# Kernel tuning notes

Measured on AMD Instinct MI355X. Metric: run time of the kernel, lower is better.

Reference implementation:

```python
import jax, jax.numpy as jnp
import numpy as np


def _graph_conv(x, src, dst, W_rel, b_rel, W_root):
    # PyG GraphConv (aggr='add'): out = lin_rel(sum_{j->i} x_j) + lin_root(x_i)
    agg = jax.ops.segment_sum(x[src], dst, num_segments=x.shape[0])  # [N, d]
    return agg @ W_rel + b_rel + x @ W_root


def setup_inputs() -> dict:
    N, E, D, H, G = 50000, 800000, 128, 128, 256
    key = jax.random.key(0)
    ks = jax.random.split(key, 24)
    x = jax.random.normal(ks[0], (N, D), dtype=jnp.float32)
    edge_index = jax.random.randint(ks[1], (2, E), 0, N, dtype=jnp.int64)
    batch = jnp.sort(jax.random.randint(ks[2], (N,), 0, G, dtype=jnp.int64))
    inp = {"x": x, "edge_index": edge_index, "batch": batch, "num_graphs": G}
    dims = [(D, H), (H, H), (H, H), (H, H), (H, H)]
    for i, (din, dout) in enumerate(dims, 1):
        s = 1.0 / np.sqrt(din)
        inp[f"W_rel{i}"] = jax.random.normal(ks[3 * i], (din, dout), dtype=jnp.float32) * s
        inp[f"b_rel{i}"] = jax.random.normal(ks[3 * i + 1], (dout,), dtype=jnp.float32) * s
        inp[f"W_root{i}"] = jax.random.normal(ks[3 * i + 2], (din, dout), dtype=jnp.float32) * s
    inp["fc1_W"] = jax.random.normal(ks[18], (H, H), dtype=jnp.float32) / np.sqrt(H)
    inp["fc1_b"] = jax.random.normal(ks[19], (H,), dtype=jnp.float32) / np.sqrt(H)
    inp["fc2_W"] = jax.random.normal(ks[20], (H, 1), dtype=jnp.float32) / np.sqrt(H)
    inp["fc2_b"] = jax.random.normal(ks[21], (1,), dtype=jnp.float32) / np.sqrt(H)
    return inp


def reference(x, edge_index, batch, num_graphs,
              W_rel1, b_rel1, W_root1,
              W_rel2, b_rel2, W_root2,
              W_rel3, b_rel3, W_root3,
              W_rel4, b_rel4, W_root4,
              W_rel5, b_rel5, W_root5,
              fc1_W, fc1_b, fc2_W, fc2_b):
    src, dst = edge_index[0], edge_index[1]
    h = x
    for Wr, br, Wl in ((W_rel1, b_rel1, W_root1), (W_rel2, b_rel2, W_root2),
                       (W_rel3, b_rel3, W_root3), (W_rel4, b_rel4, W_root4),
                       (W_rel5, b_rel5, W_root5)):
        h = jax.nn.relu(_graph_conv(h, src, dst, Wr, br, Wl))
    # global_add_pool -> [num_graphs, H]
    g = jax.ops.segment_sum(h, batch, num_segments=num_graphs)
    g = jax.nn.relu(g @ fc1_W + fc1_b)
    # dropout is identity in eval mode
    return g @ fc2_W + fc2_b  # [num_graphs, 1]
```

## Files before the change

### kernel.cpp

```cpp
#include <hip/hip_runtime.h>
#include <hip/hip_bf16.h>

typedef __attribute__((ext_vector_type(4))) float f32x4;
typedef __attribute__((ext_vector_type(8))) _Float16 f16x8;
typedef __attribute__((ext_vector_type(4))) _Float16 f16x4;

#define CHUNK 4096
#define BSH 7
#define CAP 4096


__global__ __launch_bounds__(256) void cvt_kernel(const float* __restrict__ x,
                                                  _Float16* __restrict__ hp, int N) {
  int i = blockIdx.x * blockDim.x + threadIdx.x;
  if (i < N * 32) {
    int r = i >> 5, jg = i & 31;
    float4 v = *(const float4*)(x + (size_t)r * 128 + jg * 4);
    f16x4 o = {(_Float16)v.x, (_Float16)v.y, (_Float16)v.z, (_Float16)v.w};
    int plane = jg >> 3, wc = (jg & 7) * 4;
    *(f16x4*)(hp + (size_t)plane * N * 32 + (size_t)r * 32 + wc) = o;
  }
}

__global__ __launch_bounds__(256) void bhist_kernel(const int* __restrict__ dst,
                                                    int* __restrict__ blkhist, int E, int nb) {
  __shared__ int l[512];
  int t = threadIdx.x;
  for (int i = t; i < 512; i += 256) l[i] = 0;
  __syncthreads();
  int cbase = blockIdx.x * CHUNK;
  #pragma unroll
  for (int i = 0; i < CHUNK / 256; ++i) {
    int idx = cbase + i * 256 + t;
    if (idx < E) atomicAdd(&l[dst[idx] >> BSH], 1);
  }
  __syncthreads();
  for (int i = t; i < 512; i += 256) blkhist[blockIdx.x * 512 + i] = l[i];
}

__global__ __launch_bounds__(512) void bscan_kernel(const int* __restrict__ blkhist, int nblk,
                                                    int* __restrict__ base,
                                                    int* __restrict__ gcursor, int nb, int E) {
  __shared__ int wsum[8], wpre[8];
  int t = threadIdx.x, lane = t & 63, w = t >> 6;
  int v = 0;
  int b = 0;
  for (; b + 4 <= nblk; b += 4)
    v += blkhist[b * 512 + t] + blkhist[(b + 1) * 512 + t] +
         blkhist[(b + 2) * 512 + t] + blkhist[(b + 3) * 512 + t];
  for (; b < nblk; ++b) v += blkhist[b * 512 + t];
  int incl = v;
  #pragma unroll
  for (int o = 1; o < 64; o <<= 1) {
    int x = __shfl_up(incl, o, 64);
    if (lane >= o) incl += x;
  }
  if (lane == 63) wsum[w] = incl;
  __syncthreads();
  if (t == 0) {
    int run = 0;
    #pragma unroll
    for (int q = 0; q < 8; ++q) { wpre[q] = run; run += wsum[q]; }
  }
  __syncthreads();
  int excl = wpre[w] + incl - v;
  if (t < nb) { base[t] = excl; gcursor[t] = excl; }
  if (t == 0) base[nb] = E;
}

__global__ __launch_bounds__(256) void bscatter_kernel(const int* __restrict__ src,
                                                       const int* __restrict__ dst,
                                                       int* __restrict__ gcursor,
                                                       int2* __restrict__ pairs, int E, int nb) {
  __shared__ int lcnt[512], lstart[512], lpos[512], lgbase[512];
  __shared__ int2 lp[CHUNK];
  __shared__ int wsum[4], wpre[4];
  int t = threadIdx.x, lane = t & 63, w = t >> 6;
  for (int i = t; i < 512; i += 256) lcnt[i] = 0;
  __syncthreads();
  int cbase = blockIdx.x * CHUNK;
  int m = E - cbase; if (m > CHUNK) m = CHUNK;
  #pragma unroll
  for (int i = 0; i < CHUNK / 256; ++i) {
    int idx = i * 256 + t;
    if (idx < m) atomicAdd(&lcnt[dst[cbase + idx] >> BSH], 1);
  }
  __syncthreads();
  int c0 = lcnt[2 * t], c1 = lcnt[2 * t + 1];
  int s = c0 + c1, incl = s;
  #pragma unroll
  for (int o = 1; o < 64; o <<= 1) {
    int x = __shfl_up(incl, o, 64);
    if (lane >= o) incl += x;
  }
  if (lane == 63) wsum[w] = incl;
  __syncthreads();
  if (t == 0) {
    int run = 0;
    #pragma unroll
    for (int q = 0; q < 4; ++q) { wpre[q] = run; run += wsum[q]; }
  }
  __syncthreads();
  int excl = wpre[w] + incl - s;
  lstart[2 * t] = excl;          lpos[2 * t] = excl;
  lstart[2 * t + 1] = excl + c0; lpos[2 * t + 1] = excl + c0;
  if (2 * t < nb && c0 > 0) lgbase[2 * t] = atomicAdd(&gcursor[2 * t], c0);
  if (2 * t + 1 < nb && c1 > 0) lgbase[2 * t + 1] = atomicAdd(&gcursor[2 * t + 1], c1);
  __syncthreads();
  #pragma unroll
  for (int i = 0; i < CHUNK / 256; ++i) {
    int idx = i * 256 + t;
    if (idx < m) {
      int d = dst[cbase + idx], sv = src[cbase + idx];
      int p = atomicAdd(&lpos[d >> BSH], 1);
      lp[p] = make_int2(sv, d);
    }
  }
  __syncthreads();
  for (int i = t; i < m; i += 256) {
    int2 pr = lp[i];
    int b = pr.y >> BSH;
    pairs[lgbase[b] + (i - lstart[b])] = pr;
  }
}

__global__ __launch_bounds__(256) void bbuild_kernel(const int2* __restrict__ pairs,
                                                     const int* __restrict__ base,
                                                     int* __restrict__ row_ptr,
                                                     int* __restrict__ col, int N, int E) {
  __shared__ int cnt[128], cur[128], w2[2];
  __shared__ int cl[CAP];
  int b = blockIdx.x, t = threadIdx.x;
  int mb = base[b], me = base[b + 1], m = me - mb;
  if (t < 128) cnt[t] = 0;
  __syncthreads();
  for (int i = t; i < m; i += 256) atomicAdd(&cnt[pairs[mb + i].y & 127], 1);
  __syncthreads();
  int v = 0, incl = 0;
  if (t < 128) {
    v = cnt[t]; incl = v;
    #pragma unroll
    for (int o = 1; o < 64; o <<= 1) {
      int x = __shfl_up(incl, o, 64);
      if ((t & 63) >= o) incl += x;
    }
    if ((t & 63) == 63) w2[t >> 6] = incl;
  }
  __syncthreads();
  if (t < 128) {
    int excl = incl - v + ((t & 64) ? w2[0] : 0);
    cur[t] = excl;
    int node = (b << BSH) + t;
    if (node < N) row_ptr[node] = mb + excl;
  }
  if (b == 0 && t == 0) row_ptr[N] = E;
  __syncthreads();
  if (m <= CAP) {
    for (int i = t; i < m; i += 256) {
      int2 p = pairs[mb + i];
      int pos = atomicAdd(&cur[p.y & 127], 1);
      cl[pos] = p.x;
    }
    __syncthreads();
    for (int i = t; i < m; i += 256) col[mb + i] = cl[i];
  } else {
    for (int i = t; i < m; i += 256) {
      int2 p = pairs[mb + i];
      int pos = atomicAdd(&cur[p.y & 127], 1);
      col[mb + pos] = p.x;
    }
  }
}

struct W10 { const float* p[10]; };

__global__ __launch_bounds__(256) void prep_kernel(W10 wp, _Float16* __restrict__ Whi,
                                                   _Float16* __restrict__ Wlo, float wscale) {
  int l = blockIdx.x >> 7;
  int idx = (blockIdx.x & 127) * 256 + threadIdx.x;
  int col = idx >> 8;
  int k = idx & 255;
  const float* __restrict__ Wrel = wp.p[l];
  const float* __restrict__ Wroot = wp.p[5 + l];
  float v = (k < 128) ? Wrel[k * 128 + col] : Wroot[(k - 128) * 128 + col];
  v *= wscale;
  _Float16 hi = (_Float16)v;
  _Float16 lo = (_Float16)(v - (float)hi);
  Whi[(size_t)l * 32768 + idx] = hi;
  Wlo[(size_t)l * 32768 + idx] = lo;
}

__global__ __launch_bounds__(256) void spmm_kernel(const _Float16* __restrict__ hplanes,
                                                   const int* __restrict__ row_ptr,
                                                   const int* __restrict__ col,
                                                   _Float16* __restrict__ aggplanes,
                                                   int N, int nbpp) {
  int pass = blockIdx.x / nbpp;
  int blk = blockIdx.x - pass * nbpp;
  int t = threadIdx.x;
  int quad = t >> 2, lq = t & 3;
  int row = blk * 64 + quad;
  if (row >= N) return;
  size_t planeN = (size_t)N * 32;
  const char* __restrict__ hb = (const char*)(hplanes + (size_t)pass * planeN);
  unsigned lofs = (unsigned)lq << 4;
  int s = row_ptr[row], e = row_ptr[row + 1];
  float acc[8];
  #pragma unroll
  for (int q = 0; q < 8; ++q) acc[q] = 0.f;
  if (s < e) {
    int c[8];
    #pragma unroll
    for (int q = 0; q < 8; ++q) { int x = s + q; c[q] = col[x < e ? x : e - 1]; }
    int i = s;
    for (; i + 8 <= e; i += 8) {
      f16x8 v[8];
      #pragma unroll
      for (int q = 0; q < 8; ++q) v[q] = *(const f16x8*)(hb + ((((unsigned)c[q]) << 6) | lofs));
      #pragma unroll
      for (int q = 0; q < 8; ++q) { int x = i + 8 + q; c[q] = col[x < e ? x : e - 1]; }
      #pragma unroll
      for (int z = 0; z < 8; ++z)
        acc[z] += (((float)v[0][z] + (float)v[1][z]) + ((float)v[2][z] + (float)v[3][z])) +
                  (((float)v[4][z] + (float)v[5][z]) + ((float)v[6][z] + (float)v[7][z]));
    }
    if (i < e) {
      f16x8 v[8];
      #pragma unroll
      for (int q = 0; q < 8; ++q) v[q] = *(const f16x8*)(hb + ((((unsigned)c[q]) << 6) | lofs));
      #pragma unroll
      for (int q = 0; q < 8; ++q) {
        float m = (i + q < e) ? 1.f : 0.f;
        #pragma unroll
        for (int z = 0; z < 8; ++z) acc[z] = fmaf(m, (float)v[q][z], acc[z]);
      }
    }
  }
  f16x8 o;
  #pragma unroll
  for (int q = 0; q < 8; ++q) o[q] = (_Float16)acc[q];
  *(f16x8*)(aggplanes + (size_t)pass * planeN + (size_t)row * 32 + lq * 8) = o;
}

__global__ __launch_bounds__(256) void gemm_kernel(const _Float16* __restrict__ aggp,
                                                   const _Float16* __restrict__ hp,
                                                   const _Float16* __restrict__ Whi,
                                                   const _Float16* __restrict__ Wlo,
                                                   const float* __restrict__ bias,
                                                   float bscale,
                                                   _Float16* __restrict__ outp, int N) {
  size_t planeN = (size_t)N * 32;
  int wv = threadIdx.x >> 6;
  int lane = threadIdx.x & 63;
  int l16 = lane & 15;
  int khalf = lane >> 4;
  int koff = khalf * 8;
  int row_base = blockIdx.x * 64;
  int col_base = wv * 32;

  f32x4 acc[4][2];
  #pragma unroll
  for (int r = 0; r < 4; r++)
    #pragma unroll
    for (int c = 0; c < 2; c++) acc[r][c] = (f32x4){0.f, 0.f, 0.f, 0.f};

  #pragma unroll
  for (int ks = 0; ks < 8; ++ks) {
    int k0 = ks * 32;
    const _Float16* Abase = (ks < 4) ? (aggp + (size_t)ks * planeN)
                                     : (hp + (size_t)(ks - 4) * planeN);
    f16x8 bh[2], bl[2];
    #pragma unroll
    for (int c = 0; c < 2; c++) {
      int col = col_base + c * 16 + l16;
      bh[c] = *(const f16x8*)(Whi + col * 256 + k0 + koff);
      bl[c] = *(const f16x8*)(Wlo + col * 256 + k0 + koff);
    }
    #pragma unroll
    for (int r = 0; r < 4; r++) {
      int row = row_base + r * 16 + l16;
      if (row >= N) row = N - 1;
      f16x8 a = *(const f16x8*)(Abase + (size_t)row * 32 + koff);
      #pragma unroll
      for (int c = 0; c < 2; c++) {
        acc[r][c] = __builtin_amdgcn_mfma_f32_16x16x32_f16(a, bh[c], acc[r][c], 0, 0, 0);
        acc[r][c] = __builtin_amdgcn_mfma_f32_16x16x32_f16(a, bl[c], acc[r][c], 0, 0, 0);
      }
    }
  }

  #pragma unroll
  for (int r = 0; r < 4; r++) {
    #pragma unroll
    for (int c = 0; c < 2; c++) {
      int cc = col_base + c * 16 + l16;
      float b = bias[cc] * bscale;
      #pragma unroll
      for (int tt = 0; tt < 4; tt++) {
        int row = row_base + r * 16 + khalf * 4 + tt;
        if (row < N) {
          float v = acc[r][c][tt] + b;
          outp[(size_t)wv * planeN + (size_t)row * 32 + (c * 16 + l16)] =
              (_Float16)(v > 0.f ? v : 0.f);
        }
      }
    }
  }
}

static __device__ __forceinline__ int lbound(const int* __restrict__ a, int n, int v) {
  int lo = 0, hi = n;
  while (lo < hi) {
    int m = (lo + hi) >> 1;
    if (a[m] < v) lo = m + 1; else hi = m;
  }
  return lo;
}

__global__ __launch_bounds__(128) void poolhead_kernel(const _Float16* __restrict__ h,
                                                       const int* __restrict__ batch,
                                                       const float* __restrict__ fc1W,
                                                       const float* __restrict__ fc1b,
                                                       const float* __restrict__ fc2W,
                                                       const float* __restrict__ fc2b,
                                                       float* __restrict__ out, int N,
                                                       float unscale) {
  int gid = blockIdx.x, j = threadIdx.x;
  int start = lbound(batch, N, gid);
  int end = lbound(batch, N, gid + 1);
  size_t planeN = (size_t)N * 32;
  const _Float16* __restrict__ base = h + (size_t)(j >> 5) * planeN + (j & 31);
  float acc = 0.f;
  int r = start;
  for (; r + 3 < end; r += 4) {
    acc += (float)base[(size_t)r * 32] + (float)base[(size_t)(r + 1) * 32] +
           (float)base[(size_t)(r + 2) * 32] + (float)base[(size_t)(r + 3) * 32];
  }
  for (; r < end; ++r) acc += (float)base[(size_t)r * 32];
  __shared__ float grow[128];
  __shared__ float red[128];
  grow[j] = acc * unscale;
  __syncthreads();
  float a1 = fc1b[j];
  #pragma unroll 8
  for (int k = 0; k < 128; ++k) a1 = fmaf(grow[k], fc1W[k * 128 + j], a1);
  a1 = a1 > 0.f ? a1 : 0.f;
  red[j] = a1 * fc2W[j];
  __syncthreads();
  #pragma unroll
  for (int s2 = 64; s2 > 0; s2 >>= 1) {
    if (j < s2) red[j] += red[j + s2];
    __syncthreads();
  }
  if (j == 0) out[gid] = red[0] + fc2b[0];
}

extern "C" void kernel_launch(void* const* d_in, const int* in_sizes, int n_in,
                              void* d_out, int out_size, void* d_ws, size_t ws_size,
                              hipStream_t stream) {
  const float* x = (const float*)d_in[0];
  const int* edge = (const int*)d_in[1];
  const int* batch = (const int*)d_in[2];
  const int N = in_sizes[0] / 128;
  const int E = in_sizes[1] / 2;
  const int G = out_size;
  const int* esrc = edge;
  const int* edst = edge + E;
  const int NB = (N + 127) >> BSH;
  const int nb1 = (E + CHUNK - 1) / CHUNK;

  char* ws = (char*)d_ws;
  size_t off = 0;
  auto alloc = [&](size_t bytes) -> void* {
    void* p = ws + off;
    off = (off + bytes + 255) & ~(size_t)255;
    return p;
  };
  _Float16* x16  = (_Float16*)alloc((size_t)N * 128 * 2);
  _Float16* bufA = (_Float16*)alloc((size_t)N * 128 * 2);
  _Float16* bufB = (_Float16*)alloc((size_t)N * 128 * 2);
  _Float16* agg  = (_Float16*)alloc((size_t)N * 128 * 2);
  _Float16* Whi  = (_Float16*)alloc((size_t)5 * 32768 * 2);
  _Float16* Wlo  = (_Float16*)alloc((size_t)5 * 32768 * 2);
  int* row_ptr   = (int*)alloc((size_t)(N + 1) * 4);
  int* col       = (int*)alloc((size_t)E * 4);
  int2* pairs    = (int2*)alloc((size_t)E * 8);
  int* blkhist   = (int*)alloc((size_t)nb1 * 512 * 4);
  int* base      = (int*)alloc(520 * 4);
  int* gcursor   = (int*)alloc(512 * 4);
  if (off > ws_size) return;

  bhist_kernel<<<nb1, 256, 0, stream>>>(edst, blkhist, E, NB);
  bscan_kernel<<<1, 512, 0, stream>>>(blkhist, nb1, base, gcursor, NB, E);
  bscatter_kernel<<<nb1, 256, 0, stream>>>(esrc, edst, gcursor, pairs, E, NB);
  bbuild_kernel<<<NB, 256, 0, stream>>>(pairs, base, row_ptr, col, N, E);

  cvt_kernel<<<(N * 32 + 255) / 256, 256, 0, stream>>>(x, x16, N);

  const float S = 8.0f;
  W10 wp;
  for (int l = 0; l < 5; ++l) {
    wp.p[l] = (const float*)d_in[4 + 3 * l];
    wp.p[5 + l] = (const float*)d_in[6 + 3 * l];
  }
  prep_kernel<<<640, 256, 0, stream>>>(wp, Whi, Wlo, 1.0f / S);

  const _Float16* hin = x16;
  _Float16* hout = bufA;
  int nbpp = (N + 63) / 64;
  int gemm_grid = (N + 63) / 64;
  float bscale = 1.0f;
  for (int l = 0; l < 5; ++l) {
    bscale /= S;
    spmm_kernel<<<4 * nbpp, 256, 0, stream>>>(hin, row_ptr, col, agg, N, nbpp);
    gemm_kernel<<<gemm_grid, 256, 0, stream>>>(agg, hin,
                                               Whi + (size_t)l * 32768, Wlo + (size_t)l * 32768,
                                               (const float*)d_in[5 + 3 * l], bscale, hout, N);
    hin = hout;
    hout = (hout == bufA) ? bufB : bufA;
  }
  poolhead_kernel<<<G, 128, 0, stream>>>(hin, batch,
                                         (const float*)d_in[19], (const float*)d_in[20],
                                         (const float*)d_in[21], (const float*)d_in[22],
                                         (float*)d_out, N, 32768.0f);
}
```

Baseline: 372.1 us.

## Sort SpMM rows by in-degree to balance work within wavefronts

Builds a degree histogram during CSR construction, scans it, and scatters rows into a degree-bucketed permutation with cached row ranges. The SpMM kernel then walks rows in permuted order, so rows in the same wavefront have similar edge counts and less divergence. The cost is three extra setup launches plus a memset, and the output writes become scattered rather than contiguous.

```diff
diff --git a/kernel.cpp b/kernel.cpp
--- a/kernel.cpp
+++ b/kernel.cpp
@@ -127,7 +127,8 @@
 __global__ __launch_bounds__(256) void bbuild_kernel(const int2* __restrict__ pairs,
                                                      const int* __restrict__ base,
                                                      int* __restrict__ row_ptr,
-                                                     int* __restrict__ col, int N, int E) {
+                                                     int* __restrict__ col,
+                                                     int* __restrict__ dcnt, int N, int E) {
   __shared__ int cnt[128], cur[128], w2[2];
   __shared__ int cl[CAP];
   int b = blockIdx.x, t = threadIdx.x;
@@ -151,7 +152,10 @@
     int excl = incl - v + ((t & 64) ? w2[0] : 0);
     cur[t] = excl;
     int node = (b << BSH) + t;
-    if (node < N) row_ptr[node] = mb + excl;
+    if (node < N) {
+      row_ptr[node] = mb + excl;
+      atomicAdd(&dcnt[v < 63 ? v : 63], 1);
+    }
   }
   if (b == 0 && t == 0) row_ptr[N] = E;
   __syncthreads();
@@ -169,6 +173,33 @@
       int pos = atomicAdd(&cur[p.y & 127], 1);
       col[mb + pos] = p.x;
     }
+  }
+}
+
+__global__ void dscan_kernel(const int* __restrict__ dcnt, int* __restrict__ dcur) {
+  int t = threadIdx.x;
+  int v = dcnt[t];
+  int incl = v;
+  #pragma unroll
+  for (int o = 1; o < 64; o <<= 1) {
+    int x = __shfl_up(incl, o, 64);
+    if (t >= o) incl += x;
+  }
+  dcur[t] = incl - v;
+}
+
+__global__ __launch_bounds__(256) void dscatter_kernel(const int* __restrict__ row_ptr,
+                                                       int* __restrict__ dcur,
+                                                       int* __restrict__ perm,
+                                                       int2* __restrict__ prange, int N) {
+  int r = blockIdx.x * 256 + threadIdx.x;
+  if (r < N) {
+    int s = row_ptr[r], e = row_ptr[r + 1];
+    int deg = e - s;
+    int b = deg < 63 ? deg : 63;
+    int pos = atomicAdd(&dcur[b], 1);
+    perm[pos] = r;
+    prange[pos] = make_int2(s, e);
   }
 }
 
@@ -191,7 +222,8 @@
 }
 
 __global__ __launch_bounds__(256) void spmm_kernel(const _Float16* __restrict__ hplanes,
-                                                   const int* __restrict__ row_ptr,
+                                                   const int* __restrict__ perm,
+                                                   const int2* __restrict__ prange,
                                                    const int* __restrict__ col,
                                                    _Float16* __restrict__ aggplanes,
                                                    int N, int nbpp) {
@@ -199,12 +231,14 @@
   int blk = blockIdx.x - pass * nbpp;
   int t = threadIdx.x;
   int quad = t >> 2, lq = t & 3;
-  int row = blk * 64 + quad;
-  if (row >= N) return;
+  int qi = blk * 64 + quad;
+  if (qi >= N) return;
+  int row = perm[qi];
+  int2 se = prange[qi];
   size_t planeN = (size_t)N * 32;
   const char* __restrict__ hb = (const char*)(hplanes + (size_t)pass * planeN);
   unsigned lofs = (unsigned)lq << 4;
-  int s = row_ptr[row], e = row_ptr[row + 1];
+  int s = se.x, e = se.y;
   float acc[8];
   #pragma unroll
   for (int q = 0; q < 8; ++q) acc[q] = 0.f;
@@ -388,12 +422,20 @@
   int* blkhist   = (int*)alloc((size_t)nb1 * 512 * 4);
   int* base      = (int*)alloc(520 * 4);
   int* gcursor   = (int*)alloc(512 * 4);
+  int* dcnt      = (int*)alloc(64 * 4);
+  int* dcur      = (int*)alloc(64 * 4);
+  int* perm      = (int*)alloc((size_t)N * 4);
+  int2* prange   = (int2*)alloc((size_t)N * 8);
   if (off > ws_size) return;
+
+  hipMemsetAsync(dcnt, 0, 64 * 4, stream);
 
   bhist_kernel<<<nb1, 256, 0, stream>>>(edst, blkhist, E, NB);
   bscan_kernel<<<1, 512, 0, stream>>>(blkhist, nb1, base, gcursor, NB, E);
   bscatter_kernel<<<nb1, 256, 0, stream>>>(esrc, edst, gcursor, pairs, E, NB);
-  bbuild_kernel<<<NB, 256, 0, stream>>>(pairs, base, row_ptr, col, N, E);
+  bbuild_kernel<<<NB, 256, 0, stream>>>(pairs, base, row_ptr, col, dcnt, N, E);
+  dscan_kernel<<<1, 64, 0, stream>>>(dcnt, dcur);
+  dscatter_kernel<<<(N + 255) / 256, 256, 0, stream>>>(row_ptr, dcur, perm, prange, N);
 
   cvt_kernel<<<(N * 32 + 255) / 256, 256, 0, stream>>>(x, x16, N);
 
@@ -412,7 +454,7 @@
   float bscale = 1.0f;
   for (int l = 0; l < 5; ++l) {
     bscale /= S;
-    spmm_kernel<<<4 * nbpp, 256, 0, stream>>>(hin, row_ptr, col, agg, N, nbpp);
+    spmm_kernel<<<4 * nbpp, 256, 0, stream>>>(hin, perm, prange, col, agg, N, nbpp);
     gemm_kernel<<<gemm_grid, 256, 0, stream>>>(agg, hin,
                                                Whi + (size_t)l * 32768, Wlo + (size_t)l * 32768,
                                                (const float*)d_in[5 + 3 * l], bscale, hout, N);
```

Result: slower. 674.0 us (+81.1%).
